# Performance work log

Measured on AMD Instinct MI355X. Metric: run time of the kernel, lower is better.

The kernel has to match this reference:

```python
import jax, jax.numpy as jnp
import numpy as np

N_NODES = 100000
N_EDGES = 1600000
IN_DIM = 128
OUT_DIM = 32
N_HEADS = 4


def setup_inputs() -> dict:
    key = jax.random.key(0)
    k1, k2, k3, k4, k5 = jax.random.split(key, 5)
    x = jax.random.normal(k1, (N_NODES, IN_DIM), dtype=jnp.float32)
    edge_index = jax.random.randint(k2, (2, N_EDGES), 0, N_NODES, dtype=jnp.int64)
    # torch nn.Linear weight layout: [out_features, in_features]
    W = jax.random.normal(k3, (OUT_DIM * N_HEADS, IN_DIM), dtype=jnp.float32) * (1.0 / np.sqrt(IN_DIM))
    a_left = jax.random.normal(k4, (N_HEADS, OUT_DIM), dtype=jnp.float32) * 0.01
    a_right = jax.random.normal(k5, (N_HEADS, OUT_DIM), dtype=jnp.float32) * 0.01
    return {"x": x, "edge_index": edge_index, "W": W, "a_left": a_left, "a_right": a_right}


def reference(x, edge_index, W, a_left, a_right):
    N = x.shape[0]
    H, D = a_left.shape
    # h: [N, H, D]
    h = (x @ W.T).reshape(N, H, D)
    src = edge_index[0]
    dst = edge_index[1]
    h_src = h[src]                                   # [E, H, D] gather
    h_dst = h[dst]                                   # [E, H, D] gather
    e = jnp.einsum('ehd,hd->eh', h_src, a_left) + jnp.einsum('ehd,hd->eh', h_dst, a_right)
    e = jax.nn.leaky_relu(e, negative_slope=0.2)
    e_exp = jnp.exp(e)                               # faithful: no max-subtraction, as in source
    denom = jax.ops.segment_sum(e_exp, dst, num_segments=N)   # [N, H]
    alpha = e_exp / (denom[dst] + 1e-8)              # [E, H]
    weighted = h_src * alpha[:, :, None]             # [E, H, D]
    out = jax.ops.segment_sum(weighted, dst, num_segments=N)  # [N, H, D]
    return out.reshape(N, H * D)                     # concat=True
```

## Files before the change

### kernel.cpp

```cpp
#include <hip/hip_runtime.h>
#include <hip/hip_bf16.h>


constexpr int IN_DIM = 128;
constexpr int HD     = 128;
constexpr int CSHIFT = 9;
constexpr int CCAP   = 9216;
constexpr int CPAD   = 16;
constexpr int WCOLS  = 144;

typedef float f32x4 __attribute__((ext_vector_type(4)));
typedef short short8 __attribute__((ext_vector_type(8)));

__device__ __forceinline__ unsigned short f2bf(float f) {
  __hip_bfloat16 b = __float2bfloat16(f);
  return *(unsigned short*)&b;
}
__device__ __forceinline__ float bfl(unsigned u) { return __uint_as_float(u << 16); }
__device__ __forceinline__ float bfh(unsigned u) { return __uint_as_float(u & 0xffff0000u); }

__global__ __launch_bounds__(1024)
void prep_k(const float* __restrict__ W, const float* __restrict__ a_left,
            const float* __restrict__ a_right,
            unsigned short* __restrict__ Whb, unsigned short* __restrict__ Wlb,
            int* __restrict__ ccnt) {
  const int t = threadIdx.x;
  for (int i = t; i < 256 * CPAD; i += 1024) ccnt[i] = 0;

  for (int i = t; i < 128 * 128; i += 1024) {
    float w = W[i];
    unsigned wu = __float_as_uint(w);
    unsigned short h = (unsigned short)(wu >> 16);
    float hf = __uint_as_float(wu & 0xffff0000u);
    Whb[i] = h;
    Wlb[i] = f2bf(w - hf);
  }
  {
    int vec = t >> 7;
    int k   = t & 127;
    int hd  = vec & 3;
    const float* av = (vec < 4) ? a_left : a_right;
    float s = 0.f;
    for (int d = 0; d < 32; ++d) s += av[hd * 32 + d] * W[(hd * 32 + d) * IN_DIM + k];
    unsigned su = __float_as_uint(s);
    unsigned short h = (unsigned short)(su >> 16);
    float hf = __uint_as_float(su & 0xffff0000u);
    Whb[(128 + vec) * 128 + k] = h;
    Wlb[(128 + vec) * 128 + k] = f2bf(s - hf);
  }
  for (int i = t; i < 8 * 128; i += 1024) {
    Whb[136 * 128 + i] = 0;
    Wlb[136 * 128 + i] = 0;
  }
}

__device__ __forceinline__
void gemm_role(char* xs, int gb_idx,
               const float* __restrict__ x,
               const unsigned short* __restrict__ Whb,
               const unsigned short* __restrict__ Wlb,
               unsigned int* __restrict__ hb,
               float* __restrict__ el, float* __restrict__ er, int N) {
  const int tid  = threadIdx.x;
  const int lane = tid & 63;
  const int wv   = tid >> 6;
  const int lcol = lane & 15;
  const int lk   = lane >> 4;
  const int n0   = gb_idx * 64;

#pragma unroll
  for (int i = 0; i < 8; ++i) {
    int f  = tid + 256 * i;
    int r  = f >> 5;
    int c4 = f & 31;
    int node = n0 + r;
    float4 v = make_float4(0.f, 0.f, 0.f, 0.f);
    if (node < N) v = *(const float4*)&x[(size_t)node * IN_DIM + c4 * 4];
    float vf[4] = {v.x, v.y, v.z, v.w};
    unsigned short hs[4], ls[4];
#pragma unroll
    for (int j = 0; j < 4; ++j) {
      unsigned xu = __float_as_uint(vf[j]);
      hs[j] = (unsigned short)(xu >> 16);
      float hf = __uint_as_float(xu & 0xffff0000u);
      ls[j] = f2bf(vf[j] - hf);
    }
    int sw = (c4 * 8) ^ ((r & 7) << 4);
    uint2 ph = make_uint2((unsigned)hs[0] | ((unsigned)hs[1] << 16),
                          (unsigned)hs[2] | ((unsigned)hs[3] << 16));
    uint2 pl = make_uint2((unsigned)ls[0] | ((unsigned)ls[1] << 16),
                          (unsigned)ls[2] | ((unsigned)ls[3] << 16));
    *(uint2*)&xs[r * 256 + sw]         = ph;
    *(uint2*)&xs[16384 + r * 256 + sw] = pl;
  }
  __syncthreads();

  f32x4 acc[4][2];
  f32x4 acc2[4];
#pragma unroll
  for (int rt = 0; rt < 4; ++rt) {
    acc[rt][0] = (f32x4){0.f, 0.f, 0.f, 0.f};
    acc[rt][1] = (f32x4){0.f, 0.f, 0.f, 0.f};
    acc2[rt]   = (f32x4){0.f, 0.f, 0.f, 0.f};
  }

#pragma unroll
  for (int ks = 0; ks < 4; ++ks) {
    const int kb = ks * 32 + lk * 8;
    short8 bh0 = *(const short8*)&Whb[(size_t)(wv * 32 + lcol) * 128 + kb];
    short8 bl0 = *(const short8*)&Wlb[(size_t)(wv * 32 + lcol) * 128 + kb];
    short8 bh1 = *(const short8*)&Whb[(size_t)(wv * 32 + 16 + lcol) * 128 + kb];
    short8 bl1 = *(const short8*)&Wlb[(size_t)(wv * 32 + 16 + lcol) * 128 + kb];
    short8 bh2 = {}, bl2 = {};
    if (wv == 0) {
      bh2 = *(const short8*)&Whb[(size_t)(128 + lcol) * 128 + kb];
      bl2 = *(const short8*)&Wlb[(size_t)(128 + lcol) * 128 + kb];
    }
#pragma unroll
    for (int rt = 0; rt < 4; ++rt) {
      int row = rt * 16 + lcol;
      int kbyte = ks * 64 + lk * 16;
      int ad  = row * 256 + (kbyte ^ ((row & 7) << 4));
      short8 ah = *(const short8*)&xs[ad];
      short8 al = *(const short8*)&xs[16384 + ad];
      acc[rt][0] = __builtin_amdgcn_mfma_f32_16x16x32_bf16(ah, bh0, acc[rt][0], 0, 0, 0);
      acc[rt][0] = __builtin_amdgcn_mfma_f32_16x16x32_bf16(ah, bl0, acc[rt][0], 0, 0, 0);
      acc[rt][0] = __builtin_amdgcn_mfma_f32_16x16x32_bf16(al, bh0, acc[rt][0], 0, 0, 0);
      acc[rt][1] = __builtin_amdgcn_mfma_f32_16x16x32_bf16(ah, bh1, acc[rt][1], 0, 0, 0);
      acc[rt][1] = __builtin_amdgcn_mfma_f32_16x16x32_bf16(ah, bl1, acc[rt][1], 0, 0, 0);
      acc[rt][1] = __builtin_amdgcn_mfma_f32_16x16x32_bf16(al, bh1, acc[rt][1], 0, 0, 0);
      if (wv == 0) {
        acc2[rt] = __builtin_amdgcn_mfma_f32_16x16x32_bf16(ah, bh2, acc2[rt], 0, 0, 0);
        acc2[rt] = __builtin_amdgcn_mfma_f32_16x16x32_bf16(ah, bl2, acc2[rt], 0, 0, 0);
        acc2[rt] = __builtin_amdgcn_mfma_f32_16x16x32_bf16(al, bh2, acc2[rt], 0, 0, 0);
      }
    }
  }

#pragma unroll
  for (int rt = 0; rt < 4; ++rt) {
#pragma unroll
    for (int ct = 0; ct < 2; ++ct) {
      float av[4] = {acc[rt][ct][0], acc[rt][ct][1], acc[rt][ct][2], acc[rt][ct][3]};
      float pt[4];
#pragma unroll
      for (int r = 0; r < 4; ++r) pt[r] = __shfl_xor(av[r], 1, 64);
      int col = wv * 32 + ct * 16 + lcol;
      int nb  = n0 + rt * 16 + lk * 4;
      if (!(lane & 1)) {
#pragma unroll
        for (int r = 0; r < 4; ++r) {
          int node = nb + r;
          if (node < N)
            hb[(size_t)node * 64 + (col >> 1)] =
                (unsigned)f2bf(av[r]) | ((unsigned)f2bf(pt[r]) << 16);
        }
      }
    }
    if (wv == 0 && lcol < 8) {
      float* dstp = (lcol < 4) ? el : er;
      int hd = lcol & 3;
      int nb = n0 + rt * 16 + lk * 4;
#pragma unroll
      for (int r = 0; r < 4; ++r) {
        int node = nb + r;
        if (node < N) dstp[node * 4 + hd] = acc2[rt][r];
      }
    }
  }
}

__device__ __forceinline__
void binA_role(char* smem, int ab_idx,
               const int* __restrict__ ei, int* __restrict__ ccnt,
               unsigned* __restrict__ c1buf, int E, int ncb) {
  unsigned*       staged = (unsigned*)smem;
  unsigned short* sbin   = (unsigned short*)(smem + 8192);
  int*            hist   = (int*)(smem + 12288);
  int*            loff   = (int*)(smem + 13312);
  int*            cur    = (int*)(smem + 14336);
  int*            gbase  = (int*)(smem + 15360);
  int*            lws    = (int*)(smem + 16384);
  const int t = threadIdx.x;
  const int base = ab_idx * 2048;

  hist[t] = 0;
  __syncthreads();

  int src[8], dst[8], bin[8];
#pragma unroll
  for (int i = 0; i < 8; ++i) {
    int e = base + t + 256 * i;
    if (e < E) {
      src[i] = __builtin_nontemporal_load(&ei[e]);
      dst[i] = __builtin_nontemporal_load(&ei[E + e]);
      bin[i] = dst[i] >> CSHIFT;
      atomicAdd(&hist[bin[i]], 1);
    } else bin[i] = -1;
  }
  __syncthreads();

  int v = hist[t], s = v;
#pragma unroll
  for (int d = 1; d < 64; d <<= 1) {
    int u = __shfl_up(s, d, 64);
    if ((t & 63) >= d) s += u;
  }
  if ((t & 63) == 63) lws[t >> 6] = s;
  __syncthreads();
  int prefix = 0;
  for (int i = 0; i < (t >> 6); ++i) prefix += lws[i];
  int excl = prefix + s - v;
  loff[t] = excl;
  cur[t]  = excl;
  gbase[t] = (t < ncb && v > 0) ? atomicAdd(&ccnt[t * CPAD], v) : 0;
  __syncthreads();

#pragma unroll
  for (int i = 0; i < 8; ++i) {
    if (bin[i] >= 0) {
      int p = atomicAdd(&cur[bin[i]], 1);
      staged[p] = (unsigned)src[i] | ((unsigned)(dst[i] & 511) << 17);
      sbin[p]   = (unsigned short)bin[i];
    }
  }
  __syncthreads();

  const int tot = loff[255] + hist[255];
  for (int j = t; j < tot; j += 256) {
    int b = sbin[j];
    int pos = gbase[b] + (j - loff[b]);
    if (pos < CCAP) c1buf[(size_t)b * CCAP + pos] = staged[j];
  }
}

__global__ __launch_bounds__(256)
void fused_k(const float* __restrict__ x,
             const unsigned short* __restrict__ Whb,
             const unsigned short* __restrict__ Wlb,
             unsigned int* __restrict__ hb, float* __restrict__ el,
             float* __restrict__ er, const int* __restrict__ ei,
             int* __restrict__ ccnt, unsigned* __restrict__ c1buf,
             int N, int E, int ncb, int nab) {
  __shared__ __align__(16) char smem[32768];
  const int k = blockIdx.x;
  const int twoA = 2 * nab;
  if (k < twoA && (k & 1)) {
    binA_role(smem, k >> 1, ei, ccnt, c1buf, E, ncb);
  } else {
    int gidx = (k < twoA) ? (k >> 1) : (k - nab);
    gemm_role(smem, gidx, x, Whb, Wlb, hb, el, er, N);
  }
}

__global__ __launch_bounds__(512)
void binB_k(const unsigned* __restrict__ c1buf, const int* __restrict__ ccnt,
            int* __restrict__ offsets, int* __restrict__ csr,
            int N, int ncb, int E) {
  __shared__ int hist[512];
  __shared__ int wsum[8];
  __shared__ int lws2[4];
  __shared__ int sgb;
  const int b = blockIdx.x, t = threadIdx.x;

  hist[t] = 0;

  int cv = 0, cs = 0;
  if (t < 256) {
    cv = (t < ncb) ? ccnt[t * CPAD] : 0;
    cs = cv;
#pragma unroll
    for (int d = 1; d < 64; d <<= 1) {
      int u = __shfl_up(cs, d, 64);
      if ((t & 63) >= d) cs += u;
    }
    if ((t & 63) == 63) lws2[t >> 6] = cs;
  }
  if (t == 0 && b == 0) offsets[N] = E;
  __syncthreads();
  if (t < 256) {
    int cpre = 0;
    for (int i = 0; i < (t >> 6); ++i) cpre += lws2[i];
    if (t == b) sgb = cpre + cs - cv;
  }
  __syncthreads();
  const int gb = sgb;

  int m = ccnt[b * CPAD];
  if (m > CCAP) m = CCAP;
  const unsigned* bp = c1buf + (size_t)b * CCAP;
  for (int i = t; i < m; i += 512) atomicAdd(&hist[bp[i] >> 17], 1);
  __syncthreads();

  int v = hist[t], s = v;
#pragma unroll
  for (int d = 1; d < 64; d <<= 1) {
    int u = __shfl_up(s, d, 64);
    if ((t & 63) >= d) s += u;
  }
  if ((t & 63) == 63) wsum[t >> 6] = s;
  __syncthreads();
  int prefix = 0;
  for (int w = 0; w < (t >> 6); ++w) prefix += wsum[w];
  int excl = prefix + s - v;
  int node = (b << CSHIFT) + t;
  if (node < N) offsets[node] = gb + excl;
  hist[t] = excl;
  __syncthreads();

  for (int i = t; i < m; i += 512) {
    unsigned u = bp[i];
    int r = atomicAdd(&hist[u >> 17], 1);
    csr[gb + r] = (int)(u & 0x1FFFFu);
  }
}

__global__ __launch_bounds__(256)
void agg_k(const char* __restrict__ hbc, const char* __restrict__ elc,
           const float* __restrict__ er, const int* __restrict__ offsets,
           const int* __restrict__ csr, float* __restrict__ out, int N) {
  const int wid  = (blockIdx.x * blockDim.x + threadIdx.x) >> 6;
  const int lane = threadIdx.x & 63;
  if (wid >= N) return;
  const int start = offsets[wid];
  const int end   = offsets[wid + 1];
  const int q    = lane >> 4;
  const int ql   = lane & 15;
  const int head = ql >> 2;
  const unsigned qoff = (unsigned)(ql << 4);
  const unsigned hoff = (unsigned)(head << 2);
  const float erv = er[wid * 4 + head];

  float a0=0.f,a1=0.f,a2=0.f,a3=0.f,a4=0.f,a5=0.f,a6=0.f,a7=0.f,den=0.f;

  for (int base = start; base < end; base += 64) {
    int lim = end - base; if (lim > 64) lim = 64;
    int ce  = base + lane;
    int creg = __builtin_nontemporal_load(&csr[(ce < end) ? ce : (end - 1)]);

    int i = 0;
    for (; i + 16 <= lim; i += 16) {
      int s0 = __shfl(creg, i + q, 64);
      int s1 = __shfl(creg, i + 4 + q, 64);
      int s2 = __shfl(creg, i + 8 + q, 64);
      int s3 = __shfl(creg, i + 12 + q, 64);
      uint4 h0 = *(const uint4*)(hbc + (((unsigned)s0 << 8) + qoff));
      uint4 h1 = *(const uint4*)(hbc + (((unsigned)s1 << 8) + qoff));
      uint4 h2 = *(const uint4*)(hbc + (((unsigned)s2 << 8) + qoff));
      uint4 h3 = *(const uint4*)(hbc + (((unsigned)s3 << 8) + qoff));
      float e0 = *(const float*)(elc + (((unsigned)s0 << 4) + hoff));
      float e1 = *(const float*)(elc + (((unsigned)s1 << 4) + hoff));
      float e2 = *(const float*)(elc + (((unsigned)s2 << 4) + hoff));
      float e3 = *(const float*)(elc + (((unsigned)s3 << 4) + hoff));
      float t0 = e0 + erv; t0 = (t0 > 0.f) ? t0 : 0.2f * t0;
      float t1 = e1 + erv; t1 = (t1 > 0.f) ? t1 : 0.2f * t1;
      float t2 = e2 + erv; t2 = (t2 > 0.f) ? t2 : 0.2f * t2;
      float t3 = e3 + erv; t3 = (t3 > 0.f) ? t3 : 0.2f * t3;
      float w0 = __expf(t0), w1 = __expf(t1), w2 = __expf(t2), w3 = __expf(t3);
      a0 += w0 * bfl(h0.x) + w1 * bfl(h1.x) + w2 * bfl(h2.x) + w3 * bfl(h3.x);
      a1 += w0 * bfh(h0.x) + w1 * bfh(h1.x) + w2 * bfh(h2.x) + w3 * bfh(h3.x);
      a2 += w0 * bfl(h0.y) + w1 * bfl(h1.y) + w2 * bfl(h2.y) + w3 * bfl(h3.y);
      a3 += w0 * bfh(h0.y) + w1 * bfh(h1.y) + w2 * bfh(h2.y) + w3 * bfh(h3.y);
      a4 += w0 * bfl(h0.z) + w1 * bfl(h1.z) + w2 * bfl(h2.z) + w3 * bfl(h3.z);
      a5 += w0 * bfh(h0.z) + w1 * bfh(h1.z) + w2 * bfh(h2.z) + w3 * bfh(h3.z);
      a6 += w0 * bfl(h0.w) + w1 * bfl(h1.w) + w2 * bfl(h2.w) + w3 * bfl(h3.w);
      a7 += w0 * bfh(h0.w) + w1 * bfh(h1.w) + w2 * bfh(h2.w) + w3 * bfh(h3.w);
      den += w0 + w1 + w2 + w3;
    }
    if (i + 8 <= lim) {
      int s0 = __shfl(creg, i + q, 64);
      int s1 = __shfl(creg, i + 4 + q, 64);
      uint4 h0 = *(const uint4*)(hbc + (((unsigned)s0 << 8) + qoff));
      uint4 h1 = *(const uint4*)(hbc + (((unsigned)s1 << 8) + qoff));
      float e0 = *(const float*)(elc + (((unsigned)s0 << 4) + hoff));
      float e1 = *(const float*)(elc + (((unsigned)s1 << 4) + hoff));
      float t0 = e0 + erv; t0 = (t0 > 0.f) ? t0 : 0.2f * t0;
      float t1 = e1 + erv; t1 = (t1 > 0.f) ? t1 : 0.2f * t1;
      float w0 = __expf(t0), w1 = __expf(t1);
      a0 += w0 * bfl(h0.x) + w1 * bfl(h1.x);
      a1 += w0 * bfh(h0.x) + w1 * bfh(h1.x);
      a2 += w0 * bfl(h0.y) + w1 * bfl(h1.y);
      a3 += w0 * bfh(h0.y) + w1 * bfh(h1.y);
      a4 += w0 * bfl(h0.z) + w1 * bfl(h1.z);
      a5 += w0 * bfh(h0.z) + w1 * bfh(h1.z);
      a6 += w0 * bfl(h0.w) + w1 * bfl(h1.w);
      a7 += w0 * bfh(h0.w) + w1 * bfh(h1.w);
      den += w0 + w1;
      i += 8;
    }
    if (i < lim) {
      int i0 = i + q, i1 = i + 4 + q;
      int s0 = __shfl(creg, (i0 < lim) ? i0 : 0, 64);
      int s1 = __shfl(creg, (i1 < lim) ? i1 : 0, 64);
      uint4 h0 = *(const uint4*)(hbc + (((unsigned)s0 << 8) + qoff));
      uint4 h1 = *(const uint4*)(hbc + (((unsigned)s1 << 8) + qoff));
      float e0 = *(const float*)(elc + (((unsigned)s0 << 4) + hoff));
      float e1 = *(const float*)(elc + (((unsigned)s1 << 4) + hoff));
      float t0 = e0 + erv; t0 = (t0 > 0.f) ? t0 : 0.2f * t0;
      float t1 = e1 + erv; t1 = (t1 > 0.f) ? t1 : 0.2f * t1;
      float w0 = __expf(t0), w1 = __expf(t1);
      if (i0 >= lim) w0 = 0.f;
      if (i1 >= lim) w1 = 0.f;
      a0 += w0 * bfl(h0.x) + w1 * bfl(h1.x);
      a1 += w0 * bfh(h0.x) + w1 * bfh(h1.x);
      a2 += w0 * bfl(h0.y) + w1 * bfl(h1.y);
      a3 += w0 * bfh(h0.y) + w1 * bfh(h1.y);
      a4 += w0 * bfl(h0.z) + w1 * bfl(h1.z);
      a5 += w0 * bfh(h0.z) + w1 * bfh(h1.z);
      a6 += w0 * bfl(h0.w) + w1 * bfl(h1.w);
      a7 += w0 * bfh(h0.w) + w1 * bfh(h1.w);
      den += w0 + w1;
    }
  }

#pragma unroll
  for (int m = 16; m < 64; m <<= 1) {
    a0 += __shfl_xor(a0, m, 64);  a1 += __shfl_xor(a1, m, 64);
    a2 += __shfl_xor(a2, m, 64);  a3 += __shfl_xor(a3, m, 64);
    a4 += __shfl_xor(a4, m, 64);  a5 += __shfl_xor(a5, m, 64);
    a6 += __shfl_xor(a6, m, 64);  a7 += __shfl_xor(a7, m, 64);
    den += __shfl_xor(den, m, 64);
  }
  if (q == 0) {
    float inv = 1.f / (den + 1e-8f);
    f32x4 o0 = {a0 * inv, a1 * inv, a2 * inv, a3 * inv};
    f32x4 o1 = {a4 * inv, a5 * inv, a6 * inv, a7 * inv};
    __builtin_nontemporal_store(o0, (f32x4*)&out[(size_t)wid * HD + 8 * ql]);
    __builtin_nontemporal_store(o1, (f32x4*)&out[(size_t)wid * HD + 8 * ql + 4]);
  }
}

extern "C" void kernel_launch(void* const* d_in, const int* in_sizes, int n_in,
                              void* d_out, int out_size, void* d_ws, size_t ws_size,
                              hipStream_t stream) {
  const float* x       = (const float*)d_in[0];
  const int*   ei      = (const int*)d_in[1];
  const float* W       = (const float*)d_in[2];
  const float* a_left  = (const float*)d_in[3];
  const float* a_right = (const float*)d_in[4];
  float* out = (float*)d_out;

  const int N = in_sizes[0] / IN_DIM;
  const int E = in_sizes[1] / 2;
  const int NCB = (N + (1 << CSHIFT) - 1) >> CSHIFT;
  const int GB  = (N + 63) / 64;
  const int AB  = (E + 2047) / 2048;

  char* p = (char*)d_ws;
  unsigned int* hb = (unsigned int*)p; p += (size_t)N * 64 * sizeof(unsigned int);
  float* el      = (float*)p; p += (size_t)N * 4 * sizeof(float);
  float* er      = (float*)p; p += (size_t)N * 4 * sizeof(float);
  int*   offsets = (int*)p;   p += (size_t)(N + 4) * sizeof(int);
  int*   ccnt    = (int*)p;   p += (size_t)256 * CPAD * sizeof(int);
  unsigned short* Whb = (unsigned short*)p; p += (size_t)WCOLS * 128 * sizeof(unsigned short);
  unsigned short* Wlb = (unsigned short*)p; p += (size_t)WCOLS * 128 * sizeof(unsigned short);
  int*   csr     = (int*)p;   p += (size_t)E * sizeof(int);
  unsigned* c1buf = (unsigned*)p; p += (size_t)NCB * CCAP * sizeof(unsigned);

  prep_k<<<1, 1024, 0, stream>>>(W, a_left, a_right, Whb, Wlb, ccnt);
  fused_k<<<GB + AB, 256, 0, stream>>>(x, Whb, Wlb, hb, el, er,
                                       ei, ccnt, c1buf, N, E, NCB, AB);
  binB_k<<<NCB, 512, 0, stream>>>(c1buf, ccnt, offsets, csr, N, NCB, E);
  agg_k<<<(N + 3) / 4, 256, 0, stream>>>((const char*)hb, (const char*)el, er,
                                         offsets, csr, out, N);
}
```

Measured before the change: 231.8 us.

## Run edge binning pass A standalone and fuse pass B with GEMM blocks

Moves the first binning pass (edge scatter into coarse bins) out of the GEMM-fused kernel into its own launch. The second binning pass (per-bin CSR build) is folded into the GEMM kernel instead, as interleaved blocks that now use 256 threads with two histogram entries per thread. The goal is to overlap the CSR build with the projection GEMM and keep the same number of kernel launches. In exchange, binA no longer overlaps with the GEMM, and only 196 binB blocks run beside the GEMM blocks, so load balance may be worse.

Measured after the change: 244.4 us. 1.05x slower.

```diff
diff --git a/kernel.cpp b/kernel.cpp
--- a/kernel.cpp
+++ b/kernel.cpp
@@ -51,6 +51,66 @@
   for (int i = t; i < 8 * 128; i += 1024) {
     Whb[136 * 128 + i] = 0;
     Wlb[136 * 128 + i] = 0;
+  }
+}
+
+__global__ __launch_bounds__(256)
+void binA_k(const int* __restrict__ ei, int* __restrict__ ccnt,
+            unsigned* __restrict__ c1buf, int E, int ncb) {
+  __shared__ unsigned staged[2048];
+  __shared__ unsigned short sbin[2048];
+  __shared__ int hist[256], loff[256], cur[256], gbase[256];
+  __shared__ int lws[4];
+  const int t = threadIdx.x;
+  const int base = blockIdx.x * 2048;
+
+  hist[t] = 0;
+  __syncthreads();
+
+  int src[8], dst[8], bin[8];
+#pragma unroll
+  for (int i = 0; i < 8; ++i) {
+    int e = base + t + 256 * i;
+    if (e < E) {
+      src[i] = __builtin_nontemporal_load(&ei[e]);
+      dst[i] = __builtin_nontemporal_load(&ei[E + e]);
+      bin[i] = dst[i] >> CSHIFT;
+      atomicAdd(&hist[bin[i]], 1);
+    } else bin[i] = -1;
+  }
+  __syncthreads();
+
+  int v = hist[t], s = v;
+#pragma unroll
+  for (int d = 1; d < 64; d <<= 1) {
+    int u = __shfl_up(s, d, 64);
+    if ((t & 63) >= d) s += u;
+  }
+  if ((t & 63) == 63) lws[t >> 6] = s;
+  __syncthreads();
+  int prefix = 0;
+  for (int i = 0; i < (t >> 6); ++i) prefix += lws[i];
+  int excl = prefix + s - v;
+  loff[t] = excl;
+  cur[t]  = excl;
+  gbase[t] = (t < ncb && v > 0) ? atomicAdd(&ccnt[t * CPAD], v) : 0;
+  __syncthreads();
+
+#pragma unroll
+  for (int i = 0; i < 8; ++i) {
+    if (bin[i] >= 0) {
+      int p = atomicAdd(&cur[bin[i]], 1);
+      staged[p] = (unsigned)src[i] | ((unsigned)(dst[i] & 511) << 17);
+      sbin[p]   = (unsigned short)bin[i];
+    }
+  }
+  __syncthreads();
+
+  const int tot = loff[255] + hist[255];
+  for (int j = t; j < tot; j += 256) {
+    int b = sbin[j];
+    int pos = gbase[b] + (j - loff[b]);
+    if (pos < CCAP) c1buf[(size_t)b * CCAP + pos] = staged[j];
   }
 }
 
@@ -171,147 +231,90 @@
 }
 
 __device__ __forceinline__
-void binA_role(char* smem, int ab_idx,
-               const int* __restrict__ ei, int* __restrict__ ccnt,
-               unsigned* __restrict__ c1buf, int E, int ncb) {
-  unsigned*       staged = (unsigned*)smem;
-  unsigned short* sbin   = (unsigned short*)(smem + 8192);
-  int*            hist   = (int*)(smem + 12288);
-  int*            loff   = (int*)(smem + 13312);
-  int*            cur    = (int*)(smem + 14336);
-  int*            gbase  = (int*)(smem + 15360);
-  int*            lws    = (int*)(smem + 16384);
+void binB_role(char* smem, int b,
+               const unsigned* __restrict__ c1buf, const int* __restrict__ ccnt,
+               int* __restrict__ offsets, int* __restrict__ csr,
+               int N, int ncb, int E) {
+  int* hist = (int*)smem;
+  int* cur  = hist + 512;
+  int* wsum = cur + 512;
+  int* lws2 = wsum + 4;
+  int* sgb  = lws2 + 4;
   const int t = threadIdx.x;
-  const int base = ab_idx * 2048;
+  const int w = t >> 6;
 
   hist[t] = 0;
-  __syncthreads();
-
-  int src[8], dst[8], bin[8];
-#pragma unroll
-  for (int i = 0; i < 8; ++i) {
-    int e = base + t + 256 * i;
-    if (e < E) {
-      src[i] = __builtin_nontemporal_load(&ei[e]);
-      dst[i] = __builtin_nontemporal_load(&ei[E + e]);
-      bin[i] = dst[i] >> CSHIFT;
-      atomicAdd(&hist[bin[i]], 1);
-    } else bin[i] = -1;
-  }
-  __syncthreads();
-
-  int v = hist[t], s = v;
+  hist[t + 256] = 0;
+
+  int cv = (t < ncb) ? ccnt[t * CPAD] : 0;
+  int cs = cv;
+#pragma unroll
+  for (int d = 1; d < 64; d <<= 1) {
+    int u = __shfl_up(cs, d, 64);
+    if ((t & 63) >= d) cs += u;
+  }
+  if ((t & 63) == 63) lws2[w] = cs;
+  if (t == 0 && b == 0) offsets[N] = E;
+  __syncthreads();
+  {
+    int cpre = 0;
+    for (int i = 0; i < w; ++i) cpre += lws2[i];
+    if (t == b) *sgb = cpre + cs - cv;
+  }
+  __syncthreads();
+  const int gb = *sgb;
+
+  int m = ccnt[b * CPAD];
+  if (m > CCAP) m = CCAP;
+  const unsigned* bp = c1buf + (size_t)b * CCAP;
+  for (int i = t; i < m; i += 256) atomicAdd(&hist[bp[i] >> 17], 1);
+  __syncthreads();
+
+  int v0 = hist[2 * t], v1 = hist[2 * t + 1];
+  int ps = v0 + v1;
+  int s = ps;
 #pragma unroll
   for (int d = 1; d < 64; d <<= 1) {
     int u = __shfl_up(s, d, 64);
     if ((t & 63) >= d) s += u;
   }
-  if ((t & 63) == 63) lws[t >> 6] = s;
-  __syncthreads();
-  int prefix = 0;
-  for (int i = 0; i < (t >> 6); ++i) prefix += lws[i];
-  int excl = prefix + s - v;
-  loff[t] = excl;
-  cur[t]  = excl;
-  gbase[t] = (t < ncb && v > 0) ? atomicAdd(&ccnt[t * CPAD], v) : 0;
-  __syncthreads();
-
-#pragma unroll
-  for (int i = 0; i < 8; ++i) {
-    if (bin[i] >= 0) {
-      int p = atomicAdd(&cur[bin[i]], 1);
-      staged[p] = (unsigned)src[i] | ((unsigned)(dst[i] & 511) << 17);
-      sbin[p]   = (unsigned short)bin[i];
-    }
-  }
-  __syncthreads();
-
-  const int tot = loff[255] + hist[255];
-  for (int j = t; j < tot; j += 256) {
-    int b = sbin[j];
-    int pos = gbase[b] + (j - loff[b]);
-    if (pos < CCAP) c1buf[(size_t)b * CCAP + pos] = staged[j];
+  if ((t & 63) == 63) wsum[w] = s;
+  __syncthreads();
+  int pre = 0;
+  for (int i = 0; i < w; ++i) pre += wsum[i];
+  int excl0 = gb + pre + s - ps;
+  int excl1 = excl0 + v0;
+  int node0 = (b << CSHIFT) + 2 * t;
+  if (node0 < N)     offsets[node0]     = excl0;
+  if (node0 + 1 < N) offsets[node0 + 1] = excl1;
+  cur[2 * t]     = excl0;
+  cur[2 * t + 1] = excl1;
+  __syncthreads();
+
+  for (int i = t; i < m; i += 256) {
+    unsigned u = bp[i];
+    int r = atomicAdd(&cur[u >> 17], 1);
+    csr[r] = (int)(u & 0x1FFFFu);
   }
 }
 
 __global__ __launch_bounds__(256)
-void fused_k(const float* __restrict__ x,
-             const unsigned short* __restrict__ Whb,
-             const unsigned short* __restrict__ Wlb,
-             unsigned int* __restrict__ hb, float* __restrict__ el,
-             float* __restrict__ er, const int* __restrict__ ei,
-             int* __restrict__ ccnt, unsigned* __restrict__ c1buf,
-             int N, int E, int ncb, int nab) {
+void fused2_k(const float* __restrict__ x,
+              const unsigned short* __restrict__ Whb,
+              const unsigned short* __restrict__ Wlb,
+              unsigned int* __restrict__ hb, float* __restrict__ el,
+              float* __restrict__ er,
+              const unsigned* __restrict__ c1buf, const int* __restrict__ ccnt,
+              int* __restrict__ offsets, int* __restrict__ csr,
+              int N, int E, int ncb, int nbb) {
   __shared__ __align__(16) char smem[32768];
   const int k = blockIdx.x;
-  const int twoA = 2 * nab;
-  if (k < twoA && (k & 1)) {
-    binA_role(smem, k >> 1, ei, ccnt, c1buf, E, ncb);
+  const int twoB = 2 * nbb;
+  if (k < twoB && (k & 1)) {
+    binB_role(smem, k >> 1, c1buf, ccnt, offsets, csr, N, ncb, E);
   } else {
-    int gidx = (k < twoA) ? (k >> 1) : (k - nab);
+    int gidx = (k < twoB) ? (k >> 1) : (k - nbb);
     gemm_role(smem, gidx, x, Whb, Wlb, hb, el, er, N);
-  }
-}
-
-__global__ __launch_bounds__(512)
-void binB_k(const unsigned* __restrict__ c1buf, const int* __restrict__ ccnt,
-            int* __restrict__ offsets, int* __restrict__ csr,
-            int N, int ncb, int E) {
-  __shared__ int hist[512];
-  __shared__ int wsum[8];
-  __shared__ int lws2[4];
-  __shared__ int sgb;
-  const int b = blockIdx.x, t = threadIdx.x;
-
-  hist[t] = 0;
-
-  int cv = 0, cs = 0;
-  if (t < 256) {
-    cv = (t < ncb) ? ccnt[t * CPAD] : 0;
-    cs = cv;
-#pragma unroll
-    for (int d = 1; d < 64; d <<= 1) {
-      int u = __shfl_up(cs, d, 64);
-      if ((t & 63) >= d) cs += u;
-    }
-    if ((t & 63) == 63) lws2[t >> 6] = cs;
-  }
-  if (t == 0 && b == 0) offsets[N] = E;
-  __syncthreads();
-  if (t < 256) {
-    int cpre = 0;
-    for (int i = 0; i < (t >> 6); ++i) cpre += lws2[i];
-    if (t == b) sgb = cpre + cs - cv;
-  }
-  __syncthreads();
-  const int gb = sgb;
-
-  int m = ccnt[b * CPAD];
-  if (m > CCAP) m = CCAP;
-  const unsigned* bp = c1buf + (size_t)b * CCAP;
-  for (int i = t; i < m; i += 512) atomicAdd(&hist[bp[i] >> 17], 1);
-  __syncthreads();
-
-  int v = hist[t], s = v;
-#pragma unroll
-  for (int d = 1; d < 64; d <<= 1) {
-    int u = __shfl_up(s, d, 64);
-    if ((t & 63) >= d) s += u;
-  }
-  if ((t & 63) == 63) wsum[t >> 6] = s;
-  __syncthreads();
-  int prefix = 0;
-  for (int w = 0; w < (t >> 6); ++w) prefix += wsum[w];
-  int excl = prefix + s - v;
-  int node = (b << CSHIFT) + t;
-  if (node < N) offsets[node] = gb + excl;
-  hist[t] = excl;
-  __syncthreads();
-
-  for (int i = t; i < m; i += 512) {
-    unsigned u = bp[i];
-    int r = atomicAdd(&hist[u >> 17], 1);
-    csr[gb + r] = (int)(u & 0x1FFFFu);
   }
 }
 
@@ -458,9 +461,10 @@
   unsigned* c1buf = (unsigned*)p; p += (size_t)NCB * CCAP * sizeof(unsigned);
 
   prep_k<<<1, 1024, 0, stream>>>(W, a_left, a_right, Whb, Wlb, ccnt);
-  fused_k<<<GB + AB, 256, 0, stream>>>(x, Whb, Wlb, hb, el, er,
-                                       ei, ccnt, c1buf, N, E, NCB, AB);
-  binB_k<<<NCB, 512, 0, stream>>>(c1buf, ccnt, offsets, csr, N, NCB, E);
+  binA_k<<<AB, 256, 0, stream>>>(ei, ccnt, c1buf, E, NCB);
+  fused2_k<<<GB + NCB, 256, 0, stream>>>(x, Whb, Wlb, hb, el, er,
+                                         c1buf, ccnt, offsets, csr,
+                                         N, E, NCB, NCB);
   agg_k<<<(N + 3) / 4, 256, 0, stream>>>((const char*)hb, (const char*)el, er,
                                          offsets, csr, out, N);
 }
```
